# Kernel tuning notes

Measured on AMD Instinct MI355X. Metric: run time of the kernel, lower is better.

## Reference

```python
import jax, jax.numpy as jnp
import numpy as np

N, L, D = 4096, 16, 768        # nodes, max name tokens, gpt2 embed dim
NH_NAME = 4                    # name-encoder attention heads
H, NH, NL, C = 1024, 8, 4, 16  # hidden, encoder heads, encoder layers, classes
XF = 256                       # raw node feature dim; feat_dim = XF + D = 1024
VOCAB = 50257


def _ln(x, g, b, eps=1e-5):
    m = jnp.mean(x, axis=-1, keepdims=True)
    v = jnp.var(x, axis=-1, keepdims=True)
    return (x - m) * jax.lax.rsqrt(v + eps) * g + b


def _mha(x, in_w, in_b, out_w, out_b, nh, key_mask=None):
    # x: [B, S, E]; in_w: [3E, E] (torch nn.MultiheadAttention packed qkv)
    B, S, E = x.shape
    dh = E // nh
    qkv = x @ in_w.T + in_b
    q, k, v = jnp.split(qkv, 3, axis=-1)
    q = q.reshape(B, S, nh, dh)
    k = k.reshape(B, S, nh, dh)
    v = v.reshape(B, S, nh, dh)
    scores = jnp.einsum('bqhd,bkhd->bhqk', q, k) / jnp.sqrt(jnp.asarray(dh, x.dtype))
    if key_mask is not None:
        scores = jnp.where(key_mask[:, None, None, :], scores, jnp.asarray(-1e9, x.dtype))
    a = jax.nn.softmax(scores, axis=-1)
    o = jnp.einsum('bhqk,bkhd->bqhd', a, v).reshape(B, S, E)
    return o @ out_w.T + out_b


def setup_inputs() -> dict:
    key = jax.random.key(0)
    ks = jax.random.split(key, 16)
    s = 0.02
    r = lambda i, shape: jax.random.normal(ks[i], shape, jnp.float32) * s
    return {
        'name_tokens': jax.random.randint(ks[0], (N, L), 0, VOCAB),
        'name_lens': jax.random.randint(ks[1], (N,), 1, L + 1),
        'x_feats': jax.random.normal(ks[2], (N, XF), jnp.float32),
        'wte': r(3, (VOCAB, D)),
        'mha_in_w': r(4, (3 * D, D)), 'mha_in_b': jnp.zeros((3 * D,), jnp.float32),
        'mha_out_w': r(5, (D, D)), 'mha_out_b': jnp.zeros((D,), jnp.float32),
        'bott_w': r(6, (H, XF + D)), 'bott_b': jnp.zeros((H,), jnp.float32),
        'enc_in_w': r(7, (NL, 3 * H, H)), 'enc_in_b': jnp.zeros((NL, 3 * H), jnp.float32),
        'enc_out_w': r(8, (NL, H, H)), 'enc_out_b': jnp.zeros((NL, H), jnp.float32),
        'enc_ln1_g': jnp.ones((NL, H), jnp.float32), 'enc_ln1_b': jnp.zeros((NL, H), jnp.float32),
        'enc_ln2_g': jnp.ones((NL, H), jnp.float32), 'enc_ln2_b': jnp.zeros((NL, H), jnp.float32),
        'enc_ff1_w': r(9, (NL, 2 * H, H)), 'enc_ff1_b': jnp.zeros((NL, 2 * H), jnp.float32),
        'enc_ff2_w': r(10, (NL, H, 2 * H)), 'enc_ff2_b': jnp.zeros((NL, H), jnp.float32),
        'cls_w': r(11, (C, H)), 'cls_b': jnp.zeros((C,), jnp.float32),
    }


def reference(name_tokens, name_lens, x_feats, wte,
              mha_in_w, mha_in_b, mha_out_w, mha_out_b,
              bott_w, bott_b,
              enc_in_w, enc_in_b, enc_out_w, enc_out_b,
              enc_ln1_g, enc_ln1_b, enc_ln2_g, enc_ln2_b,
              enc_ff1_w, enc_ff1_b, enc_ff2_w, enc_ff2_b,
              cls_w, cls_b):
    # --- GraphNameEncoder: batched over all N ragged name sequences ---
    mask = jnp.arange(L)[None, :] < name_lens[:, None]          # [N, L] valid-token mask
    emb = wte[name_tokens]                                      # [N, L, D]
    attn = _mha(emb, mha_in_w, mha_in_b, mha_out_w, mha_out_b, NH_NAME, key_mask=mask)
    name_emb = jnp.sum(jnp.where(mask[:, :, None], attn, 0.0), axis=1)  # [N, D]
    x = jnp.concatenate([x_feats, name_emb], axis=-1)           # [N, XF + D]
    # --- bottleneck ---
    x = x @ bott_w.T + bott_b                                   # [N, H]
    # --- TransformerEncoder on seq_len=1 (x.unsqueeze(1)), post-norm, relu ---
    h = x[:, None, :]                                           # [N, 1, H]
    for l in range(NL):
        a = _mha(h, enc_in_w[l], enc_in_b[l], enc_out_w[l], enc_out_b[l], NH)
        h = _ln(h + a, enc_ln1_g[l], enc_ln1_b[l])
        f = jax.nn.relu(h @ enc_ff1_w[l].T + enc_ff1_b[l]) @ enc_ff2_w[l].T + enc_ff2_b[l]
        h = _ln(h + f, enc_ln2_g[l], enc_ln2_b[l])
    out = h @ cls_w.T + cls_b                                   # [N, 1, C]
    return out[:, 0, :]                                         # squeeze -> [N, C]
```

## Files before the change

kernel.cpp:

```cpp
#include <hip/hip_runtime.h>

typedef unsigned short bf16_t;
typedef __attribute__((ext_vector_type(8))) __bf16 bf16x8;
typedef __attribute__((ext_vector_type(4))) float f32x4;

__device__ __forceinline__ float bf2f(unsigned v) { return __uint_as_float(v << 16); }
__device__ __forceinline__ bf16_t f2bf(float f) {
  unsigned u = __float_as_uint(f);
  return (bf16_t)((u + 0x7fffu + ((u >> 16) & 1u)) >> 16);
}
__device__ __forceinline__ unsigned pack2(float a, float b) {
  return (unsigned)f2bf(a) | ((unsigned)f2bf(b) << 16);
}

__global__ __launch_bounds__(256) void scan_lens(const int* __restrict__ lens,
                                                 int* __restrict__ offs,
                                                 int* __restrict__ Mact) {
  __shared__ int wsum[4];
  const int t = threadIdx.x;
  int v[16]; int s = 0;
#pragma unroll
  for (int i = 0; i < 16; i++) { v[i] = lens[t * 16 + i]; s += v[i]; }
  const int lane = t & 63, w = t >> 6;
  int x = s;
#pragma unroll
  for (int o = 1; o < 64; o <<= 1) {
    int y = __shfl_up(x, o);
    if (lane >= o) x += y;
  }
  if (lane == 63) wsum[w] = x;
  __syncthreads();
  int base = 0;
  for (int i = 0; i < w; i++) base += wsum[i];
  int run = base + x - s;
#pragma unroll
  for (int i = 0; i < 16; i++) { offs[t * 16 + i] = run; run += v[i]; }
  if (t == 255) Mact[0] = run;
}

__global__ void cvt_f32_bf16(const float* __restrict__ src, bf16_t* __restrict__ dst, long n4) {
  long i = (long)blockIdx.x * blockDim.x + threadIdx.x;
  if (i >= n4) return;
  float4 v = ((const float4*)src)[i];
  ((uint2*)dst)[i] = make_uint2(pack2(v.x, v.y), pack2(v.z, v.w));
}

__global__ __launch_bounds__(256) void cvt_trans(const float* __restrict__ src,
                                                 bf16_t* __restrict__ dst) {
  __shared__ float tile[32][33];
  const int l = blockIdx.z;
  const int bx = blockIdx.x * 32;
  const int by = blockIdx.y * 32;
  const float* s = src + (size_t)l * 3 * 1024 * 1024 + 2 * 1024 * 1024;
  const int tx = threadIdx.x & 31, ty = threadIdx.x >> 5;
#pragma unroll
  for (int i = 0; i < 32; i += 8)
    tile[ty + i][tx] = s[(size_t)(by + ty + i) * 1024 + bx + tx];
  __syncthreads();
  bf16_t* d = dst + (size_t)l * 1024 * 1024;
#pragma unroll
  for (int i = 0; i < 32; i += 8)
    d[(size_t)(bx + ty + i) * 1024 + by + tx] = f2bf(tile[tx][ty + i]);
}

__global__ __launch_bounds__(256) void bias_comb(const float* __restrict__ enc_out_w,
                                                 const float* __restrict__ enc_in_b,
                                                 const float* __restrict__ enc_out_b,
                                                 float* __restrict__ bc) {
  const int l = blockIdx.y;
  const int wave = threadIdx.x >> 6, lane = threadIdx.x & 63;
  const float* w = enc_out_w + (size_t)l * 1024 * 1024;
  const float* bv = enc_in_b + (size_t)l * 3072 + 2048;
  for (int c = wave; c < 16; c += 4) {
    int i = blockIdx.x * 16 + c;
    const float* wr = w + (size_t)i * 1024;
    float acc = 0.f;
    for (int j = lane; j < 1024; j += 64) acc += wr[j] * bv[j];
#pragma unroll
    for (int o = 32; o > 0; o >>= 1) acc += __shfl_down(acc, o);
    if (lane == 0) bc[(size_t)l * 1024 + i] = acc + enc_out_b[(size_t)l * 1024 + i];
  }
}

__global__ void gather_emb_c(const int* __restrict__ tok, const int* __restrict__ lens,
                             const int* __restrict__ offs, const float* __restrict__ wte,
                             bf16_t* __restrict__ emb) {
  long i = (long)blockIdx.x * blockDim.x + threadIdx.x;
  if (i >= 65536L * 192L) return;
  long nl = i / 192; int cg = (int)(i % 192);
  int n = (int)(nl >> 4), l = (int)(nl & 15);
  if (l >= lens[n]) return;
  long ro = (long)offs[n] + l;
  int t = tok[nl];
  float4 v = *(const float4*)(wte + (long)t * 768 + cg * 4);
  ((uint2*)emb)[ro * 192 + cg] = make_uint2(pack2(v.x, v.y), pack2(v.z, v.w));
}

__global__ void xfeat_lenf(const float* __restrict__ xf, const int* __restrict__ lens,
                           bf16_t* __restrict__ x, float* __restrict__ lenf) {
  long i = (long)blockIdx.x * blockDim.x + threadIdx.x;
  if (i < 4096) lenf[i] = (float)lens[i];
  if (i >= 4096L * 64L) return;
  int row = (int)(i >> 6); int c4 = (int)(i & 63) * 4;
  float4 v = *(const float4*)(xf + (long)row * 256 + c4);
  *(uint2*)(x + (long)row * 1024 + c4) = make_uint2(pack2(v.x, v.y), pack2(v.z, v.w));
}

#define BM 128
#define BN 128
#define BK 32

__device__ __forceinline__ void async16(const void* g, void* l) {
  __builtin_amdgcn_global_load_lds((const __attribute__((address_space(1))) void*)g,
                                   (__attribute__((address_space(3))) void*)l, 16, 0, 0);
}

__global__ __launch_bounds__(256, 2) void gemm_bt(
    const bf16_t* __restrict__ A, const bf16_t* __restrict__ W,
    const float* __restrict__ bias, bf16_t* __restrict__ C,
    int K, int ldc, const int* __restrict__ Mp,
    long sA, long sB, long sC) {
  const int m0 = blockIdx.y * BM;
  if (Mp != nullptr && m0 >= *Mp) return;
  __shared__ __attribute__((aligned(16))) bf16_t smem[BM * BK + BN * BK];
  bf16_t* As = smem;
  bf16_t* Bs = smem + BM * BK;
  const int t = threadIdx.x;
  const int n0 = blockIdx.x * BN;
  const int z = blockIdx.z;
  const int lane = t & 63;
  const int wr = t >> 7;
  const int wc = (t >> 6) & 1;
  const int quad = lane >> 4;
  const int r16 = lane & 15;

  f32x4 acc[4][4] = {};

  const int c0 = t, c1 = t + 256;
  const int row0 = c0 >> 2, kp0 = (c0 & 3) << 3;
  const int row1 = c1 >> 2, kp1 = (c1 & 3) << 3;
  bf16_t* lA0 = As + (size_t)(c0 & ~63) * 8;
  bf16_t* lA1 = As + (size_t)(c1 & ~63) * 8;
  bf16_t* lB0 = Bs + (size_t)(c0 & ~63) * 8;
  bf16_t* lB1 = Bs + (size_t)(c1 & ~63) * 8;
  const bf16_t* Ab = A + (size_t)z * sA + (size_t)m0 * K;
  const bf16_t* Wb = W + (size_t)z * sB + (size_t)n0 * K;
  bf16_t* Cb = C + (size_t)z * sC;

  for (int k0 = 0; k0 < K; k0 += BK) {
    __syncthreads();
    async16(Ab + (size_t)row0 * K + k0 + kp0, lA0);
    async16(Ab + (size_t)row1 * K + k0 + kp1, lA1);
    async16(Wb + (size_t)row0 * K + k0 + kp0, lB0);
    async16(Wb + (size_t)row1 * K + k0 + kp1, lB1);
    __syncthreads();
    bf16x8 af[4], bfr[4];
#pragma unroll
    for (int i = 0; i < 4; i++) {
      af[i]  = *(const bf16x8*)(As + (wr * 64 + i * 16 + r16) * BK + quad * 8);
      bfr[i] = *(const bf16x8*)(Bs + (wc * 64 + i * 16 + r16) * BK + quad * 8);
    }
#pragma unroll
    for (int i = 0; i < 4; i++)
#pragma unroll
      for (int j = 0; j < 4; j++)
        acc[i][j] = __builtin_amdgcn_mfma_f32_16x16x32_bf16(af[i], bfr[j], acc[i][j], 0, 0, 0);
  }

  __syncthreads();
  const int ldcs = 136;
  bf16_t* Cs = smem;
#pragma unroll
  for (int s = 0; s < 4; s++) {
    if (wr == (s >> 1)) {
      const int ib = (s & 1) * 2;
#pragma unroll
      for (int i2 = 0; i2 < 2; i2++) {
        const int i = ib + i2;
#pragma unroll
        for (int j = 0; j < 4; j++) {
          int col = wc * 64 + j * 16 + r16;
          float bv = bias ? bias[n0 + col] : 0.0f;
#pragma unroll
          for (int r = 0; r < 4; r++)
            Cs[(i2 * 16 + quad * 4 + r) * ldcs + col] = f2bf(acc[i][j][r] + bv);
        }
      }
    }
    __syncthreads();
    {
      const int rl = t >> 4, cl = (t & 15) * 8;
#pragma unroll
      for (int p = 0; p < 2; p++) {
        int row = rl + p * 16;
        bf16x8 v = *(const bf16x8*)(Cs + row * ldcs + cl);
        *(bf16x8*)(Cb + (size_t)(m0 + s * 32 + row) * ldc + n0 + cl) = v;
      }
    }
    __syncthreads();
  }
}

template <bool RELU>
__global__ __launch_bounds__(256, 4) void gemm128x64(
    const bf16_t* __restrict__ A, const bf16_t* __restrict__ W,
    const float* __restrict__ bias, const float* __restrict__ rowscale,
    bf16_t* __restrict__ C, int K, int ldc) {
  __shared__ __attribute__((aligned(16))) bf16_t smem[128 * 64 + 64 * 64];
  bf16_t* As = smem;
  bf16_t* Bs = smem + 128 * 64;
  const int t = threadIdx.x;
  const int m0 = blockIdx.x * 128, n0 = blockIdx.y * 64;
  const int lane = t & 63, w = t >> 6;
  const int quad = lane >> 4, r16 = lane & 15;
  f32x4 acc[2][4] = {};
  int rowA[4], kpA[4];
  bf16_t* lA[4];
#pragma unroll
  for (int i = 0; i < 4; i++) {
    int c = t + i * 256;
    rowA[i] = c >> 3;
    kpA[i] = ((c & 7) ^ (rowA[i] & 7)) << 3;
    lA[i] = As + (size_t)(c & ~63) * 8;
  }
  int rowB[2], kpB[2];
  bf16_t* lB[2];
#pragma unroll
  for (int i = 0; i < 2; i++) {
    int c = t + i * 256;
    rowB[i] = c >> 3;
    kpB[i] = ((c & 7) ^ (rowB[i] & 7)) << 3;
    lB[i] = Bs + (size_t)(c & ~63) * 8;
  }
  const bf16_t* Ab = A + (size_t)m0 * K;
  const bf16_t* Wb = W + (size_t)n0 * K;

  for (int k0 = 0; k0 < K; k0 += 64) {
    __syncthreads();
#pragma unroll
    for (int i = 0; i < 4; i++) async16(Ab + (size_t)rowA[i] * K + k0 + kpA[i], lA[i]);
#pragma unroll
    for (int i = 0; i < 2; i++) async16(Wb + (size_t)rowB[i] * K + k0 + kpB[i], lB[i]);
    __syncthreads();
#pragma unroll
    for (int kk8 = 0; kk8 < 8; kk8 += 4) {
      bf16x8 af[2], bfr[4];
#pragma unroll
      for (int i = 0; i < 2; i++) {
        int Ra = w * 32 + i * 16 + r16;
        af[i] = *(const bf16x8*)(As + Ra * 64 + (((kk8 + quad) ^ (Ra & 7)) << 3));
      }
#pragma unroll
      for (int j = 0; j < 4; j++) {
        int Rb = j * 16 + r16;
        bfr[j] = *(const bf16x8*)(Bs + Rb * 64 + (((kk8 + quad) ^ (Rb & 7)) << 3));
      }
#pragma unroll
      for (int i = 0; i < 2; i++)
#pragma unroll
        for (int j = 0; j < 4; j++)
          acc[i][j] = __builtin_amdgcn_mfma_f32_16x16x32_bf16(af[i], bfr[j], acc[i][j], 0, 0, 0);
    }
  }

  __syncthreads();
  const int ldcs = 72;
  bf16_t* Cs = smem;
#pragma unroll
  for (int i = 0; i < 2; i++) {
#pragma unroll
    for (int j = 0; j < 4; j++) {
      int col = j * 16 + r16;
      float bv = bias ? bias[n0 + col] : 0.0f;
#pragma unroll
      for (int r = 0; r < 4; r++) {
        int row = w * 32 + i * 16 + quad * 4 + r;
        float sc = rowscale ? rowscale[m0 + row] : 1.0f;
        float v = acc[i][j][r] + bv * sc;
        if (RELU) v = fmaxf(v, 0.0f);
        Cs[row * ldcs + col] = f2bf(v);
      }
    }
  }
  __syncthreads();
  {
    const int rl = t >> 3, cl = (t & 7) * 8;
#pragma unroll
    for (int p = 0; p < 4; p++) {
      int row = rl + p * 32;
      bf16x8 v = *(const bf16x8*)(Cs + row * ldcs + cl);
      *(bf16x8*)(C + (size_t)(m0 + row) * ldc + n0 + cl) = v;
    }
  }
}

__global__ __launch_bounds__(64) void attn_name(const bf16_t* __restrict__ qkv,
                                                const int* __restrict__ lens,
                                                const int* __restrict__ offs,
                                                bf16_t* __restrict__ s) {
  const int n = blockIdx.x, h = blockIdx.y;
  const int lane = threadIdx.x;
  __shared__ unsigned short qs[16][208];
  __shared__ unsigned short ks[16][208];
  __shared__ unsigned short vs[16][208];
  __shared__ float ps[16][16];
  __shared__ float wj[16];
  const int len = lens[n];
  const bf16_t* base = qkv + (size_t)offs[n] * 2304 + h * 192;
  for (int g = lane; g < len * 48; g += 64) {
    int row = g / 48, c4 = (g % 48) * 4;
    const bf16_t* p = base + (size_t)row * 2304 + c4;
    uint2 a;
    a = *(const uint2*)p;
    *(unsigned*)&qs[row][c4] = a.x; *(unsigned*)&qs[row][c4 + 2] = a.y;
    a = *(const uint2*)(p + 768);
    *(unsigned*)&ks[row][c4] = a.x; *(unsigned*)&ks[row][c4 + 2] = a.y;
    a = *(const uint2*)(p + 1536);
    *(unsigned*)&vs[row][c4] = a.x; *(unsigned*)&vs[row][c4 + 2] = a.y;
  }
  __syncthreads();
  {
    const int l = lane >> 2, j0 = (lane & 3) * 4;
    float s0 = 0, s1 = 0, s2 = 0, s3 = 0;
    for (int d = 0; d < 192; d++) {
      float q = bf2f(qs[l][d]);
      s0 += q * bf2f(ks[j0 + 0][d]);
      s1 += q * bf2f(ks[j0 + 1][d]);
      s2 += q * bf2f(ks[j0 + 2][d]);
      s3 += q * bf2f(ks[j0 + 3][d]);
    }
    const float sc = 0.07216878f;
    ps[l][j0 + 0] = s0 * sc; ps[l][j0 + 1] = s1 * sc;
    ps[l][j0 + 2] = s2 * sc; ps[l][j0 + 3] = s3 * sc;
  }
  __syncthreads();
  if (lane < 16) {
    float m = -1e30f;
    for (int j = 0; j < len; j++) m = fmaxf(m, ps[lane][j]);
    float sum = 0.f;
    for (int j = 0; j < len; j++) sum += __expf(ps[lane][j] - m);
    float inv = 1.0f / sum;
    for (int j = 0; j < 16; j++) ps[lane][j] = (j < len) ? __expf(ps[lane][j] - m) * inv : 0.0f;
  }
  __syncthreads();
  if (lane < 16) {
    float a = 0.f;
    for (int l2 = 0; l2 < len; l2++) a += ps[l2][lane];
    wj[lane] = a;
  }
  __syncthreads();
  for (int d = lane; d < 192; d += 64) {
    float a = 0.f;
    for (int j = 0; j < len; j++) a += wj[j] * bf2f(vs[j][d]);
    s[(size_t)n * 768 + h * 192 + d] = f2bf(a);
  }
}

__global__ __launch_bounds__(256) void ln_res(bf16_t* __restrict__ h, const bf16_t* __restrict__ d,
                                              const float* __restrict__ g, const float* __restrict__ b) {
  const int n = blockIdx.x, t = threadIdx.x;
  __shared__ float s1[4], s2[4];
  bf16_t* hr = h + (size_t)n * 1024;
  const bf16_t* dr = d + (size_t)n * 1024;
  float x[4];
  float sum = 0.f, ss = 0.f;
#pragma unroll
  for (int i = 0; i < 4; i++) {
    int c = t + i * 256;
    float v = bf2f(hr[c]) + bf2f(dr[c]);
    x[i] = v; sum += v; ss += v * v;
  }
#pragma unroll
  for (int o = 32; o > 0; o >>= 1) { sum += __shfl_down(sum, o); ss += __shfl_down(ss, o); }
  if ((t & 63) == 0) { s1[t >> 6] = sum; s2[t >> 6] = ss; }
  __syncthreads();
  sum = s1[0] + s1[1] + s1[2] + s1[3];
  ss  = s2[0] + s2[1] + s2[2] + s2[3];
  const float mean = sum * (1.0f / 1024.0f);
  const float var = ss * (1.0f / 1024.0f) - mean * mean;
  const float rstd = rsqrtf(var + 1e-5f);
#pragma unroll
  for (int i = 0; i < 4; i++) {
    int c = t + i * 256;
    hr[c] = f2bf((x[i] - mean) * rstd * g[c] + b[c]);
  }
}

__global__ __launch_bounds__(256) void cls_head(const bf16_t* __restrict__ h,
                                                const float* __restrict__ cw,
                                                const float* __restrict__ cb,
                                                float* __restrict__ out) {
  const int n = blockIdx.x, t = threadIdx.x, wave = t >> 6, lane = t & 63;
  const bf16_t* hr = h + (size_t)n * 1024;
  for (int c = wave; c < 16; c += 4) {
    const float* wr = cw + c * 1024;
    float acc = 0.f;
    for (int i = lane; i < 1024; i += 64) acc += bf2f(hr[i]) * wr[i];
#pragma unroll
    for (int o = 32; o > 0; o >>= 1) acc += __shfl_down(acc, o);
    if (lane == 0) out[(size_t)n * 16 + c] = acc + cb[c];
  }
}

extern "C" void kernel_launch(void* const* d_in, const int* in_sizes, int n_in,
                              void* d_out, int out_size, void* d_ws, size_t ws_size,
                              hipStream_t stream) {
  (void)in_sizes; (void)n_in; (void)out_size; (void)ws_size;
  const int* name_tokens = (const int*)d_in[0];
  const int* name_lens   = (const int*)d_in[1];
  const float* x_feats   = (const float*)d_in[2];
  const float* wte       = (const float*)d_in[3];
  const float* mha_in_w  = (const float*)d_in[4];
  const float* mha_in_b  = (const float*)d_in[5];
  const float* mha_out_w = (const float*)d_in[6];
  const float* mha_out_b = (const float*)d_in[7];
  const float* bott_w    = (const float*)d_in[8];
  const float* bott_b    = (const float*)d_in[9];
  const float* enc_in_w  = (const float*)d_in[10];
  const float* enc_in_b  = (const float*)d_in[11];
  const float* enc_out_w = (const float*)d_in[12];
  const float* enc_out_b = (const float*)d_in[13];
  const float* enc_ln1_g = (const float*)d_in[14];
  const float* enc_ln1_b = (const float*)d_in[15];
  const float* enc_ln2_g = (const float*)d_in[16];
  const float* enc_ln2_b = (const float*)d_in[17];
  const float* enc_ff1_w = (const float*)d_in[18];
  const float* enc_ff1_b = (const float*)d_in[19];
  const float* enc_ff2_w = (const float*)d_in[20];
  const float* enc_ff2_b = (const float*)d_in[21];
  const float* cls_w     = (const float*)d_in[22];
  const float* cls_b     = (const float*)d_in[23];
  float* out = (float*)d_out;

  char* base = (char*)d_ws;
  size_t off = 0;
  auto alloc = [&](size_t bytes) -> char* {
    char* p = base + off;
    off = (off + bytes + 255) & ~(size_t)255;
    return p;
  };
  bf16_t* w_qkv  = (bf16_t*)alloc((size_t)2304 * 768 * 2);
  bf16_t* w_out  = (bf16_t*)alloc((size_t)768 * 768 * 2);
  bf16_t* w_bott = (bf16_t*)alloc((size_t)1024 * 1024 * 2);
  bf16_t* w_vT   = (bf16_t*)alloc((size_t)4 * 1024 * 1024 * 2);
  bf16_t* w_enco = (bf16_t*)alloc((size_t)4 * 1024 * 1024 * 2);
  bf16_t* w_ff1  = (bf16_t*)alloc((size_t)4 * 2048 * 1024 * 2);
  bf16_t* w_ff2  = (bf16_t*)alloc((size_t)4 * 1024 * 2048 * 2);
  float*  lenf   = (float*)alloc((size_t)4096 * 4);
  int*    offs   = (int*)alloc((size_t)4096 * 4);
  int*    Mact   = (int*)alloc((size_t)256);
  char* reuse = alloc((size_t)65536 * 768 * 2);
  bf16_t* emb = (bf16_t*)reuse;
  bf16_t* s_  = (bf16_t*)reuse;
  bf16_t* x_  = (bf16_t*)(reuse + 6291456);
  bf16_t* h_  = (bf16_t*)(reuse + 6291456 + 8388608);
  bf16_t* v_  = (bf16_t*)(reuse + 6291456 + 2 * 8388608);
  bf16_t* a_  = (bf16_t*)(reuse + 6291456 + 3 * 8388608);
  bf16_t* f1_ = (bf16_t*)(reuse + 6291456 + 4 * 8388608);
  bf16_t* qkv = (bf16_t*)alloc((size_t)65536 * 2304 * 2);
  bf16_t* wc = (bf16_t*)qkv;
  float*  bc = (float*)((char*)qkv + (size_t)4 * 1024 * 1024 * 2);

  dim3 b256(256);
  auto g1 = [](long n4) { return dim3((unsigned)((n4 + 255) / 256)); };

  scan_lens<<<dim3(1), b256, 0, stream>>>(name_lens, offs, Mact);

  cvt_f32_bf16<<<g1(442368), b256, 0, stream>>>(mha_in_w, w_qkv, 442368L);
  cvt_f32_bf16<<<g1(147456), b256, 0, stream>>>(mha_out_w, w_out, 147456L);
  cvt_f32_bf16<<<g1(262144), b256, 0, stream>>>(bott_w, w_bott, 262144L);
  cvt_trans<<<dim3(32, 32, 4), b256, 0, stream>>>(enc_in_w, w_vT);
  cvt_f32_bf16<<<g1(1048576), b256, 0, stream>>>(enc_out_w, w_enco, 1048576L);
  cvt_f32_bf16<<<g1(2097152), b256, 0, stream>>>(enc_ff1_w, w_ff1, 2097152L);
  cvt_f32_bf16<<<g1(2097152), b256, 0, stream>>>(enc_ff2_w, w_ff2, 2097152L);

  gather_emb_c<<<dim3(49152), b256, 0, stream>>>(name_tokens, name_lens, offs, wte, emb);
  gemm_bt<<<dim3(18, 512), b256, 0, stream>>>(emb, w_qkv, mha_in_b, qkv, 768, 2304, Mact,
                                              0L, 0L, 0L);
  xfeat_lenf<<<dim3(1024), b256, 0, stream>>>(x_feats, name_lens, x_, lenf);
  attn_name<<<dim3(4096, 4), dim3(64), 0, stream>>>(qkv, name_lens, offs, s_);

  gemm_bt<<<dim3(8, 8, 4), b256, 0, stream>>>(
      w_enco, w_vT, (const float*)nullptr, wc, 1024, 1024, (const int*)nullptr,
      (long)1024 * 1024, (long)1024 * 1024, (long)1024 * 1024);
  bias_comb<<<dim3(64, 4), b256, 0, stream>>>(enc_out_w, enc_in_b, enc_out_b, bc);

  gemm128x64<false><<<dim3(32, 12), b256, 0, stream>>>(s_, w_out, mha_out_b, lenf,
                                                       x_ + 256, 768, 1024);
  gemm128x64<false><<<dim3(32, 16), b256, 0, stream>>>(x_, w_bott, bott_b,
                                                       (const float*)nullptr, h_, 1024, 1024);
  for (int l = 0; l < 4; l++) {
    gemm128x64<false><<<dim3(32, 16), b256, 0, stream>>>(
        h_, wc + (size_t)l * 1024 * 1024, bc + (size_t)l * 1024,
        (const float*)nullptr, a_, 1024, 1024);
    ln_res<<<dim3(4096), b256, 0, stream>>>(h_, a_, enc_ln1_g + l * 1024, enc_ln1_b + l * 1024);
    gemm128x64<true><<<dim3(32, 32), b256, 0, stream>>>(
        h_, w_ff1 + (size_t)l * 2048 * 1024, enc_ff1_b + l * 2048,
        (const float*)nullptr, f1_, 1024, 2048);
    gemm128x64<false><<<dim3(32, 16), b256, 0, stream>>>(
        f1_, w_ff2 + (size_t)l * 1024 * 2048, enc_ff2_b + l * 1024,
        (const float*)nullptr, v_, 2048, 1024);
    ln_res<<<dim3(4096), b256, 0, stream>>>(h_, v_, enc_ln2_g + l * 1024, enc_ln2_b + l * 1024);
  }
  cls_head<<<dim3(4096), b256, 0, stream>>>(h_, cls_w, cls_b, out);
}
```

Baseline: 1.209 ms.

## Double-buffer LDS tiles in both GEMM kernels to overlap loads with MFMA

Both GEMM kernels now keep two LDS tile buffers. Each iteration issues the async global-to-LDS loads for the next K tile before running MFMAs on the current one, and only one barrier per iteration remains. This aims to hide global-load latency behind matrix math instead of serialising load, barrier and compute. In exchange LDS use per block doubles, and gemm128x64 lowers its launch-bounds occupancy hint from 4 to 3 blocks per CU.

```diff
diff --git a/kernel.cpp b/kernel.cpp
--- a/kernel.cpp
+++ b/kernel.cpp
@@ -109,6 +109,7 @@
 #define BM 128
 #define BN 128
 #define BK 32
+#define SBT (BM * BK + BN * BK)
 
 __device__ __forceinline__ void async16(const void* g, void* l) {
   __builtin_amdgcn_global_load_lds((const __attribute__((address_space(1))) void*)g,
@@ -122,9 +123,7 @@
     long sA, long sB, long sC) {
   const int m0 = blockIdx.y * BM;
   if (Mp != nullptr && m0 >= *Mp) return;
-  __shared__ __attribute__((aligned(16))) bf16_t smem[BM * BK + BN * BK];
-  bf16_t* As = smem;
-  bf16_t* Bs = smem + BM * BK;
+  __shared__ __attribute__((aligned(16))) bf16_t smem[2 * SBT];
   const int t = threadIdx.x;
   const int n0 = blockIdx.x * BN;
   const int z = blockIdx.z;
@@ -139,21 +138,28 @@
   const int c0 = t, c1 = t + 256;
   const int row0 = c0 >> 2, kp0 = (c0 & 3) << 3;
   const int row1 = c1 >> 2, kp1 = (c1 & 3) << 3;
-  bf16_t* lA0 = As + (size_t)(c0 & ~63) * 8;
-  bf16_t* lA1 = As + (size_t)(c1 & ~63) * 8;
-  bf16_t* lB0 = Bs + (size_t)(c0 & ~63) * 8;
-  bf16_t* lB1 = Bs + (size_t)(c1 & ~63) * 8;
+  const size_t oc0 = (size_t)(c0 & ~63) * 8;
+  const size_t oc1 = (size_t)(c1 & ~63) * 8;
   const bf16_t* Ab = A + (size_t)z * sA + (size_t)m0 * K;
   const bf16_t* Wb = W + (size_t)z * sB + (size_t)n0 * K;
   bf16_t* Cb = C + (size_t)z * sC;
 
+  auto stage = [&](int b, int k0) {
+    bf16_t* As = smem + (size_t)b * SBT;
+    bf16_t* Bs = As + BM * BK;
+    async16(Ab + (size_t)row0 * K + k0 + kp0, As + oc0);
+    async16(Ab + (size_t)row1 * K + k0 + kp1, As + oc1);
+    async16(Wb + (size_t)row0 * K + k0 + kp0, Bs + oc0);
+    async16(Wb + (size_t)row1 * K + k0 + kp1, Bs + oc1);
+  };
+
+  stage(0, 0);
+  __syncthreads();
+  int cur = 0;
   for (int k0 = 0; k0 < K; k0 += BK) {
-    __syncthreads();
-    async16(Ab + (size_t)row0 * K + k0 + kp0, lA0);
-    async16(Ab + (size_t)row1 * K + k0 + kp1, lA1);
-    async16(Wb + (size_t)row0 * K + k0 + kp0, lB0);
-    async16(Wb + (size_t)row1 * K + k0 + kp1, lB1);
-    __syncthreads();
+    if (k0 + BK < K) stage(cur ^ 1, k0 + BK);
+    const bf16_t* As = smem + (size_t)cur * SBT;
+    const bf16_t* Bs = As + BM * BK;
     bf16x8 af[4], bfr[4];
 #pragma unroll
     for (int i = 0; i < 4; i++) {
@@ -165,9 +171,10 @@
 #pragma unroll
       for (int j = 0; j < 4; j++)
         acc[i][j] = __builtin_amdgcn_mfma_f32_16x16x32_bf16(af[i], bfr[j], acc[i][j], 0, 0, 0);
-  }
-
-  __syncthreads();
+    __syncthreads();
+    cur ^= 1;
+  }
+
   const int ldcs = 136;
   bf16_t* Cs = smem;
 #pragma unroll
@@ -201,47 +208,56 @@
   }
 }
 
+#define S64 (128 * 64 + 64 * 64)
+
 template <bool RELU>
-__global__ __launch_bounds__(256, 4) void gemm128x64(
+__global__ __launch_bounds__(256, 3) void gemm128x64(
     const bf16_t* __restrict__ A, const bf16_t* __restrict__ W,
     const float* __restrict__ bias, const float* __restrict__ rowscale,
     bf16_t* __restrict__ C, int K, int ldc) {
-  __shared__ __attribute__((aligned(16))) bf16_t smem[128 * 64 + 64 * 64];
-  bf16_t* As = smem;
-  bf16_t* Bs = smem + 128 * 64;
+  __shared__ __attribute__((aligned(16))) bf16_t smem[2 * S64];
   const int t = threadIdx.x;
   const int m0 = blockIdx.x * 128, n0 = blockIdx.y * 64;
   const int lane = t & 63, w = t >> 6;
   const int quad = lane >> 4, r16 = lane & 15;
   f32x4 acc[2][4] = {};
   int rowA[4], kpA[4];
-  bf16_t* lA[4];
+  size_t oA[4];
 #pragma unroll
   for (int i = 0; i < 4; i++) {
     int c = t + i * 256;
     rowA[i] = c >> 3;
     kpA[i] = ((c & 7) ^ (rowA[i] & 7)) << 3;
-    lA[i] = As + (size_t)(c & ~63) * 8;
+    oA[i] = (size_t)(c & ~63) * 8;
   }
   int rowB[2], kpB[2];
-  bf16_t* lB[2];
+  size_t oB[2];
 #pragma unroll
   for (int i = 0; i < 2; i++) {
     int c = t + i * 256;
     rowB[i] = c >> 3;
     kpB[i] = ((c & 7) ^ (rowB[i] & 7)) << 3;
-    lB[i] = Bs + (size_t)(c & ~63) * 8;
+    oB[i] = (size_t)(c & ~63) * 8;
   }
   const bf16_t* Ab = A + (size_t)m0 * K;
   const bf16_t* Wb = W + (size_t)n0 * K;
 
+  auto stage = [&](int b, int k0) {
+    bf16_t* As = smem + (size_t)b * S64;
+    bf16_t* Bs = As + 128 * 64;
+#pragma unroll
+    for (int i = 0; i < 4; i++) async16(Ab + (size_t)rowA[i] * K + k0 + kpA[i], As + oA[i]);
+#pragma unroll
+    for (int i = 0; i < 2; i++) async16(Wb + (size_t)rowB[i] * K + k0 + kpB[i], Bs + oB[i]);
+  };
+
+  stage(0, 0);
+  __syncthreads();
+  int cur = 0;
   for (int k0 = 0; k0 < K; k0 += 64) {
-    __syncthreads();
-#pragma unroll
-    for (int i = 0; i < 4; i++) async16(Ab + (size_t)rowA[i] * K + k0 + kpA[i], lA[i]);
-#pragma unroll
-    for (int i = 0; i < 2; i++) async16(Wb + (size_t)rowB[i] * K + k0 + kpB[i], lB[i]);
-    __syncthreads();
+    if (k0 + 64 < K) stage(cur ^ 1, k0 + 64);
+    const bf16_t* As = smem + (size_t)cur * S64;
+    const bf16_t* Bs = As + 128 * 64;
 #pragma unroll
     for (int kk8 = 0; kk8 < 8; kk8 += 4) {
       bf16x8 af[2], bfr[4];
@@ -261,9 +277,10 @@
         for (int j = 0; j < 4; j++)
           acc[i][j] = __builtin_amdgcn_mfma_f32_16x16x32_bf16(af[i], bfr[j], acc[i][j], 0, 0, 0);
     }
-  }
-
-  __syncthreads();
+    __syncthreads();
+    cur ^= 1;
+  }
+
   const int ldcs = 72;
   bf16_t* Cs = smem;
 #pragma unroll
```

New measurement: 1.213 ms. Within noise of the previous version (+0.3%).
